# Kernel tuning notes

Measured on AMD Instinct MI355X. Metric: run time of the kernel, lower is better.

The kernel has to match this reference:

```python
import jax, jax.numpy as jnp
import numpy as np
import math

N_EMBD = 1024
N_HEADS = 16
B, T = 4, 2048

def setup_inputs() -> dict:
    key = jax.random.key(0)
    k1, k2, k3 = jax.random.split(key, 3)
    x = jax.random.normal(k1, (B, T, N_EMBD), dtype=jnp.float32)
    scale = 1.0 / math.sqrt(N_EMBD)
    W_attn = jax.random.normal(k2, (N_EMBD, 3 * N_EMBD), dtype=jnp.float32) * scale
    W_proj = jax.random.normal(k3, (N_EMBD, N_EMBD), dtype=jnp.float32) * scale
    return {"x": x, "W_attn": W_attn, "W_proj": W_proj}

def reference(x, W_attn, W_proj):
    Bb, Tt, C = x.shape
    hd = C // N_HEADS
    qkv = x @ W_attn  # [B,T,3C]
    q, k, v = jnp.split(qkv, 3, axis=-1)
    # [B,H,T,hd]
    q = q.reshape(Bb, Tt, N_HEADS, hd).transpose(0, 2, 1, 3)
    k = k.reshape(Bb, Tt, N_HEADS, hd).transpose(0, 2, 1, 3)
    v = v.reshape(Bb, Tt, N_HEADS, hd).transpose(0, 2, 1, 3)
    att = jnp.einsum('bhqd,bhkd->bhqk', q, k) * (1.0 / math.sqrt(hd))
    mask = jnp.tril(jnp.ones((Tt, Tt), dtype=bool))
    att = jnp.where(mask[None, None], att, -jnp.inf)
    att = jax.nn.softmax(att, axis=-1)
    out = jnp.einsum('bhqk,bhkd->bhqd', att, v)
    out = out.transpose(0, 2, 1, 3).reshape(Bb, Tt, C)
    return out @ W_proj
```

## Files before the change

kernel.cpp:

```cpp
#include <hip/hip_runtime.h>
#include <cstddef>
#include <cstdint>

typedef __attribute__((ext_vector_type(8))) _Float16 half8;
typedef __attribute__((ext_vector_type(4))) _Float16 half4;
typedef __attribute__((ext_vector_type(4))) float f32x4;
typedef __attribute__((ext_vector_type(16))) float f32x16;

#define N_EMBD 1024
#define N_HEADS 16
#define BATCH 4
#define SEQ 2048
#define C3 3072
#define HD 64

__device__ inline uint32_t pk2(float x, float y) {
    auto h2 = __builtin_amdgcn_cvt_pkrtz(x, y);
    uint32_t u;
    __builtin_memcpy(&u, &h2, 4);
    return u;
}

__device__ inline void swap32(uint32_t& a, uint32_t& b) {
    asm volatile("v_permlane32_swap_b32 %0, %1" : "+v"(a), "+v"(b));
}

__device__ inline float exp2_hw(float x) {
    float r;
    asm("v_exp_f32 %0, %1" : "=v"(r) : "v"(x));
    return r;
}

__device__ inline void transpose_tile(const float* __restrict__ in, _Float16* __restrict__ out,
                                      int R, int Ncols, int bx, int by, int tx, int ty,
                                      int scale_below, float scl) {
    __shared__ float tile[32][33];
    int n0 = bx * 32, r0 = by * 32;
#pragma unroll
    for (int i = 0; i < 32; i += 8)
        tile[ty + i][tx] = in[(size_t)(r0 + ty + i) * Ncols + n0 + tx];
    __syncthreads();
#pragma unroll
    for (int i = 0; i < 32; i += 8) {
        int orow = n0 + ty + i;
        float f = tile[tx][ty + i];
        if (orow < scale_below) f *= scl;
        out[(size_t)orow * R + r0 + tx] = (_Float16)f;
    }
}

__global__ void prep_kernel(const float* __restrict__ x, _Float16* __restrict__ xh,
                            const float* __restrict__ Wa, _Float16* __restrict__ WaT,
                            const float* __restrict__ Wp, _Float16* __restrict__ WpT) {
    const int bid = blockIdx.x;
    const int tx = threadIdx.x & 31, ty = threadIdx.x >> 5;
    const float qscale = 0.125f * 1.44269504089f;
    if (bid < 8192) {
        int i = (bid * 256 + threadIdx.x) * 4;
        float4 v = *(const float4*)(x + i);
        half4 h;
        h[0] = (_Float16)v.x; h[1] = (_Float16)v.y; h[2] = (_Float16)v.z; h[3] = (_Float16)v.w;
        *(half4*)(xh + i) = h;
    } else if (bid < 8192 + 3072) {
        int v = bid - 8192;
        transpose_tile(Wa, WaT, N_EMBD, C3, v % 96, v / 96, tx, ty, N_EMBD, qscale);
    } else {
        int v = bid - 8192 - 3072;
        transpose_tile(Wp, WpT, N_EMBD, N_EMBD, v % 32, v / 32, tx, ty, 0, 1.0f);
    }
}

__global__ void transpose_v(const _Float16* __restrict__ qkv, _Float16* __restrict__ vT) {
    __shared__ _Float16 tile[32][36];
    int t0 = blockIdx.x * 32;
    int bhd = blockIdx.y;
    int bh = bhd >> 1, dh = bhd & 1;
    int b = bh >> 4, h = bh & 15;
    int tx = threadIdx.x, ty = threadIdx.y;
#pragma unroll
    for (int i = 0; i < 32; i += 8)
        tile[ty + i][tx] = qkv[(size_t)(b * SEQ + t0 + ty + i) * C3 + 2 * N_EMBD + h * HD + dh * 32 + tx];
    __syncthreads();
#pragma unroll
    for (int i = 0; i < 32; i += 8)
        vT[((size_t)bh * HD + dh * 32 + ty + i) * SEQ + t0 + tx] = tile[tx][ty + i];
}

__device__ inline void store1(float* p, float v) { *p = v; }
__device__ inline void store1(_Float16* p, float v) { *p = (_Float16)v; }

__global__ __launch_bounds__(512, 1) void gemm192(
    const _Float16* __restrict__ A, const _Float16* __restrict__ Bt,
    _Float16* __restrict__ C, _Float16* __restrict__ vT, int M, int N, int K) {
    __shared__ _Float16 smem[2 * 256 * 64 + 2 * 192 * 64];
    _Float16* Al0 = smem;
    _Float16* Bl0 = smem + 2 * 256 * 64;
    const int tid = threadIdx.x;
    const int lane = tid & 63, wave = tid >> 6;
    const int l15 = lane & 15, l4 = lane >> 4;
    const int wm = wave >> 2, wn = wave & 3;

    const int nwg = gridDim.x, nbx = N / 192;
    int wg = blockIdx.x;
    if ((nwg & 7) == 0) { int cpx = nwg >> 3; wg = (wg & 7) * cpx + (wg >> 3); }
    const int row0 = (wg / nbx) * 256, col0 = (wg % nbx) * 192;
    const int TAU = K >> 6;

    const int srow = tid >> 3, su = tid & 7;
    const int usrc8 = (su ^ (srow & 7)) * 8;
    auto stageAu = [&](int unit, int ts) {
        __builtin_amdgcn_global_load_lds(
            (const __attribute__((address_space(1))) void*)(A + (size_t)(row0 + unit * 64 + srow) * K + ts * 64 + usrc8),
            (__attribute__((address_space(3))) void*)(Al0 + (ts & 1) * 16384 + unit * 4096 + tid * 8), 16, 0, 0);
    };
    auto stageBu = [&](int unit, int ts) {
        __builtin_amdgcn_global_load_lds(
            (const __attribute__((address_space(1))) void*)(Bt + (size_t)(col0 + unit * 64 + srow) * K + ts * 64 + usrc8),
            (__attribute__((address_space(3))) void*)(Bl0 + (ts & 1) * 12288 + unit * 4096 + tid * 8), 16, 0, 0);
    };
    auto stageTile = [&](int ts) {
        stageAu(0, ts); stageAu(1, ts); stageAu(2, ts); stageAu(3, ts);
        stageBu(0, ts); stageBu(1, ts); stageBu(2, ts);
    };

    f32x4 acc[8][3] = {};
    stageTile(0); stageTile(1);
    asm volatile("s_waitcnt vmcnt(7)" ::: "memory");
    __builtin_amdgcn_s_barrier();

    half8 a[4][2], b[3][2];
    for (int tau = 0; tau < TAU; ++tau) {
        const _Float16* Ab = Al0 + (tau & 1) * 16384;
        const _Float16* Bb = Bl0 + (tau & 1) * 12288;
        const bool t2 = (tau + 2 < TAU);

#pragma unroll
        for (int m = 0; m < 4; ++m)
#pragma unroll
            for (int ks = 0; ks < 2; ++ks) {
                int r = wm * 128 + m * 16 + l15;
                a[m][ks] = *(const half8*)(Ab + r * 64 + (((ks * 4 + l4) ^ (r & 7)) * 8));
            }
#pragma unroll
        for (int n = 0; n < 3; ++n)
#pragma unroll
            for (int ks = 0; ks < 2; ++ks) {
                int r = wn * 48 + n * 16 + l15;
                b[n][ks] = *(const half8*)(Bb + r * 64 + (((ks * 4 + l4) ^ (r & 7)) * 8));
            }
        __builtin_amdgcn_s_barrier();
        __builtin_amdgcn_s_setprio(1);
#pragma unroll
        for (int m = 0; m < 4; ++m)
#pragma unroll
            for (int n = 0; n < 2; ++n)
#pragma unroll
                for (int ks = 0; ks < 2; ++ks)
                    acc[m][n] = __builtin_amdgcn_mfma_f32_16x16x32_f16(a[m][ks], b[n][ks], acc[m][n], 0, 0, 0);
        __builtin_amdgcn_s_setprio(0);
        __builtin_amdgcn_s_barrier();

        if (t2) { stageBu(0, tau + 2); stageBu(1, tau + 2); stageBu(2, tau + 2); }
        __builtin_amdgcn_s_barrier();
        __builtin_amdgcn_s_setprio(1);
#pragma unroll
        for (int m = 0; m < 4; ++m)
#pragma unroll
            for (int ks = 0; ks < 2; ++ks)
                acc[m][2] = __builtin_amdgcn_mfma_f32_16x16x32_f16(a[m][ks], b[2][ks], acc[m][2], 0, 0, 0);
        __builtin_amdgcn_s_setprio(0);
        __builtin_amdgcn_s_barrier();

#pragma unroll
        for (int m = 0; m < 4; ++m)
#pragma unroll
            for (int ks = 0; ks < 2; ++ks) {
                int r = wm * 128 + 64 + m * 16 + l15;
                a[m][ks] = *(const half8*)(Ab + r * 64 + (((ks * 4 + l4) ^ (r & 7)) * 8));
            }
        if (t2) { stageAu(0, tau + 2); stageAu(2, tau + 2); }
        __builtin_amdgcn_s_barrier();
        __builtin_amdgcn_s_setprio(1);
#pragma unroll
        for (int m = 0; m < 4; ++m)
#pragma unroll
            for (int n = 0; n < 2; ++n)
#pragma unroll
                for (int ks = 0; ks < 2; ++ks)
                    acc[4 + m][n] = __builtin_amdgcn_mfma_f32_16x16x32_f16(a[m][ks], b[n][ks], acc[4 + m][n], 0, 0, 0);
        __builtin_amdgcn_s_setprio(0);
        __builtin_amdgcn_s_barrier();

        if (t2) { stageAu(1, tau + 2); stageAu(3, tau + 2); }
        __builtin_amdgcn_s_barrier();
        __builtin_amdgcn_s_setprio(1);
#pragma unroll
        for (int m = 0; m < 4; ++m)
#pragma unroll
            for (int ks = 0; ks < 2; ++ks)
                acc[4 + m][2] = __builtin_amdgcn_mfma_f32_16x16x32_f16(a[m][ks], b[2][ks], acc[4 + m][2], 0, 0, 0);
        __builtin_amdgcn_s_setprio(0);
        if (tau <= TAU - 3) {
            asm volatile("s_waitcnt vmcnt(7)" ::: "memory");
        } else if (tau == TAU - 2) {
            asm volatile("s_waitcnt vmcnt(0)" ::: "memory");
        }
        __builtin_amdgcn_s_barrier();
    }

    const int vlo = 2 * N_EMBD;
    const bool fuseV = (vT != nullptr) && (col0 + 192 > vlo);
    _Float16* vbuf = smem;
#pragma unroll
    for (int mi = 0; mi < 8; ++mi)
#pragma unroll
        for (int ni = 0; ni < 3; ++ni) {
            int c = col0 + wn * 48 + ni * 16 + l15;
            int rb = wm * 128 + (mi >> 2) * 64 + (mi & 3) * 16 + l4 * 4;
            if ((vT != nullptr) && c >= vlo) {
                if (fuseV) {
                    half4 hv;
#pragma unroll
                    for (int j = 0; j < 4; ++j) hv[j] = (_Float16)acc[mi][ni][j];
                    *(half4*)(&vbuf[(c - col0) * 264 + rb]) = hv;
                }
            } else {
#pragma unroll
                for (int j = 0; j < 4; ++j)
                    store1(C + (size_t)(row0 + rb + j) * N + c, acc[mi][ni][j]);
            }
        }
    if (fuseV) {
        __syncthreads();
        const int vc0 = (col0 > vlo) ? col0 : vlo;
        const int W = col0 + 192 - vc0;
        const int nch = W * 32;
        const int bB = row0 >> 11;
        const int t0 = row0 & 2047;
        for (int ch = tid; ch < nch; ch += 512) {
            int crow = ch >> 5, ck = ch & 31;
            int c = vc0 + crow;
            half8 hv = *(const half8*)(&vbuf[(c - col0) * 264 + ck * 8]);
            int hh = (c - vlo) >> 6, dd = (c - vlo) & 63;
            *(half8*)(&vT[((size_t)(bB * 16 + hh) * 64 + dd) * SEQ + t0 + ck * 8]) = hv;
        }
    }
}

template <typename OutT>
__global__ __launch_bounds__(256, 2) void gemm_h(
    const _Float16* __restrict__ A, const _Float16* __restrict__ Bt,
    OutT* __restrict__ C, int M, int N, int K) {
    __shared__ _Float16 Al[3][128 * 32];
    __shared__ _Float16 Bl[3][128 * 32];
    const int tid = threadIdx.x;
    const int wave = tid >> 6, lane = tid & 63;
    const int l15 = lane & 15, l4 = lane >> 4;
    const int gx = gridDim.x;
    int lin = blockIdx.y * gx + blockIdx.x;
    int bcol, brow;
    if ((gx & 7) == 0) {
        int cpx = gx >> 3;
        int xcd = lin & 7;
        int idx = lin >> 3;
        bcol = xcd * cpx + idx % cpx;
        brow = idx / cpx;
    } else { bcol = blockIdx.x; brow = blockIdx.y; }
    const int row0 = brow * 128, col0 = bcol * 128;
    const int wm = wave >> 1, wn = wave & 1;
    const int TAU = K >> 5;

    auto stageT = [&](int ts, int buf) {
#pragma unroll
        for (int i = 0; i < 2; ++i) {
            int c = tid + 256 * i;
            int r = c >> 2, c8 = (c & 3) * 8;
            __builtin_amdgcn_global_load_lds(
                (const __attribute__((address_space(1))) void*)(A + (size_t)(row0 + r) * K + ts * 32 + c8),
                (__attribute__((address_space(3))) void*)(&Al[buf][(size_t)(wave * 64 + 256 * i) * 8]),
                16, 0, 0);
        }
#pragma unroll
        for (int i = 0; i < 2; ++i) {
            int c = tid + 256 * i;
            int r = c >> 2, c8 = (c & 3) * 8;
            __builtin_amdgcn_global_load_lds(
                (const __attribute__((address_space(1))) void*)(Bt + (size_t)(col0 + r) * K + ts * 32 + c8),
                (__attribute__((address_space(3))) void*)(&Bl[buf][(size_t)(wave * 64 + 256 * i) * 8]),
                16, 0, 0);
        }
    };

    f32x4 acc[4][4] = {};
    stageT(0, 0); stageT(1, 1);
    asm volatile("s_waitcnt vmcnt(4)" ::: "memory");
    __builtin_amdgcn_s_barrier();

    int cur = 0;
    for (int t = 0; t < TAU; ++t) {
        int sb = cur + 2; if (sb >= 3) sb -= 3;
        if (t + 2 < TAU) stageT(t + 2, sb);
        half8 a[4], b[4];
#pragma unroll
        for (int m = 0; m < 4; ++m)
            a[m] = *(const half8*)(&Al[cur][(wm * 64 + m * 16 + l15) * 32 + l4 * 8]);
#pragma unroll
        for (int n = 0; n < 4; ++n)
            b[n] = *(const half8*)(&Bl[cur][(wn * 64 + n * 16 + l15) * 32 + l4 * 8]);
        __builtin_amdgcn_s_setprio(1);
#pragma unroll
        for (int m = 0; m < 4; ++m)
#pragma unroll
            for (int n = 0; n < 4; ++n)
                acc[m][n] = __builtin_amdgcn_mfma_f32_16x16x32_f16(a[m], b[n], acc[m][n], 0, 0, 0);
        __builtin_amdgcn_s_setprio(0);
        if (t + 2 < TAU) {
            asm volatile("s_waitcnt vmcnt(4)" ::: "memory");
        } else if (t + 1 < TAU) {
            asm volatile("s_waitcnt vmcnt(0)" ::: "memory");
        }
        __builtin_amdgcn_s_barrier();
        ++cur; if (cur == 3) cur = 0;
    }
#pragma unroll
    for (int m = 0; m < 4; ++m)
#pragma unroll
        for (int n = 0; n < 4; ++n)
#pragma unroll
            for (int j = 0; j < 4; ++j) {
                int r = row0 + wm * 64 + m * 16 + l4 * 4 + j;
                int cc = col0 + wn * 64 + n * 16 + l15;
                store1(C + (size_t)r * N + cc, acc[m][n][j]);
            }
}

__global__ __launch_bounds__(256, 3) void attn_kernel(const _Float16* __restrict__ qkv,
                                                      const _Float16* __restrict__ vT,
                                                      _Float16* __restrict__ ao) {
    const int bid = blockIdx.x;
    const int pairp = bid >> 6;
    const int bh = bid & 63;
    const int b = bh >> 4, h = bh & 15;
    const int tid = threadIdx.x, lane = tid & 63;
    const int wave = tid >> 6;
    const int l31 = lane & 31, L = lane >> 5;

    __shared__ _Float16 Kl[3][64 * 64];
    __shared__ _Float16 Vl[3][64 * 64];
    __shared__ float l_s[4][32];

    const float NEGC = -4.0f * 1.44269504089f;

    auto stage = [&](int t, int buf) {
#pragma unroll
        for (int i = 0; i < 2; ++i) {
            int idx = tid + 256 * i;
            int key = idx >> 3;
            int d8 = ((idx & 7) ^ (key & 7)) * 8;
            __builtin_amdgcn_global_load_lds(
                (const __attribute__((address_space(1))) void*)(qkv + (size_t)(b * SEQ + t * 64 + key) * C3 + N_EMBD + h * HD + d8),
                (__attribute__((address_space(3))) void*)(&Kl[buf][idx * 8]), 16, 0, 0);
        }
#pragma unroll
        for (int i = 0; i < 2; ++i) {
            int idx = tid + 256 * i;
            int d = idx >> 3;
            int k8 = ((idx & 7) ^ (d & 7)) * 8;
            __builtin_amdgcn_global_load_lds(
                (const __attribute__((address_space(1))) void*)(vT + ((size_t)bh * HD + d) * SEQ + t * 64 + k8),
                (__attribute__((address_space(3))) void*)(&Vl[buf][idx * 8]), 16, 0, 0);
        }
    };

    const f32x16 cinit = (f32x16)(NEGC);

    for (int pass = 0; pass < 2; ++pass) {
        const int qt = pass ? (15 - pairp) : pairp;
        const int q0w = qt * 128 + wave * 32;
        const int q_g = q0w + l31;
        const int nt = 2 * qt + 2;

        stage(0, 0);
        stage(1, 1);

        half8 qb[4];
#pragma unroll
        for (int ks = 0; ks < 4; ++ks)
            qb[ks] = *(const half8*)(qkv + (size_t)(b * SEQ + q_g) * C3 + h * HD + ks * 16 + L * 8);

        f32x16 o[2];
        o[0] = (f32x16)(0.f);
        o[1] = (f32x16)(0.f);
        float ls0 = 0.f, ls1 = 0.f, ls2 = 0.f, ls3 = 0.f;

        asm volatile("s_waitcnt vmcnt(4)" ::: "memory");
        __builtin_amdgcn_s_barrier();

        int cur = 0;
        for (int t = 0; t < nt; ++t) {
            const int kv0 = t * 64;
            int sb = cur + 2; if (sb >= 3) sb -= 3;
            if (t + 2 < nt) stage(t + 2, sb);

            if (kv0 <= q0w + 31) {
                const _Float16* Kb = &Kl[cur][0];
                const _Float16* Vb = &Vl[cur][0];
                f32x16 s[2];
                __builtin_amdgcn_s_setprio(1);
#pragma unroll
                for (int kb = 0; kb < 2; ++kb) {
                    const int key = kb * 32 + l31;
                    {
                        half8 kf = *(const half8*)(Kb + key * 64 + ((L ^ (key & 7)) * 8));
                        s[kb] = __builtin_amdgcn_mfma_f32_32x32x16_f16(kf, qb[0], cinit, 0, 0, 0);
                    }
#pragma unroll
                    for (int ks = 1; ks < 4; ++ks) {
                        half8 kf = *(const half8*)(Kb + key * 64 + (((ks * 2 + L) ^ (key & 7)) * 8));
                        s[kb] = __builtin_amdgcn_mfma_f32_32x32x16_f16(kf, qb[ks], s[kb], 0, 0, 0);
                    }
                }
                __builtin_amdgcn_s_setprio(0);
                const bool needmask = (kv0 + 63 > q0w);
#pragma unroll
                for (int kb = 0; kb < 2; ++kb) {
#pragma unroll
                    for (int r = 0; r < 16; ++r) {
                        float v = exp2_hw(s[kb][r]);
                        if (needmask) {
                            int key_g = kv0 + kb * 32 + (r & 3) + 8 * (r >> 2) + 4 * L;
                            v = (key_g > q_g) ? 0.f : v;
                        }
                        s[kb][r] = v;
                        if ((r & 3) == 0) ls0 += v;
                        else if ((r & 3) == 1) ls1 += v;
                        else if ((r & 3) == 2) ls2 += v;
                        else ls3 += v;
                    }
                }
                half8 paf[4];
#pragma unroll
                for (int kb = 0; kb < 2; ++kb)
#pragma unroll
                    for (int hf = 0; hf < 2; ++hf) {
                        const int bse = hf * 8;
                        uint32_t a0 = pk2(s[kb][bse + 0], s[kb][bse + 1]);
                        uint32_t b0 = pk2(s[kb][bse + 4], s[kb][bse + 5]);
                        swap32(a0, b0);
                        uint32_t a1 = pk2(s[kb][bse + 2], s[kb][bse + 3]);
                        uint32_t b1 = pk2(s[kb][bse + 6], s[kb][bse + 7]);
                        swap32(a1, b1);
                        uint32_t w[4] = {a0, a1, b0, b1};
                        __builtin_memcpy(&paf[kb * 2 + hf], w, 16);
                    }
                __builtin_amdgcn_s_setprio(1);
#pragma unroll
                for (int ks = 0; ks < 4; ++ks) {
#pragma unroll
                    for (int db = 0; db < 2; ++db) {
                        const int d = db * 32 + l31;
                        half8 vb = *(const half8*)(Vb + d * 64 + (((ks * 2 + L) ^ (d & 7)) * 8));
                        o[db] = __builtin_amdgcn_mfma_f32_32x32x16_f16(paf[ks], vb, o[db], 0, 0, 0);
                    }
                }
                __builtin_amdgcn_s_setprio(0);
            }

            if (t + 2 < nt) {
                asm volatile("s_waitcnt vmcnt(4)" ::: "memory");
            } else if (t + 1 < nt) {
                asm volatile("s_waitcnt vmcnt(0)" ::: "memory");
            }
            __builtin_amdgcn_s_barrier();
            ++cur; if (cur == 3) cur = 0;
        }

        float lrow = (ls0 + ls1) + (ls2 + ls3);
        lrow += __shfl_xor(lrow, 32, 64);
        l_s[wave][l31] = lrow;
        asm volatile("s_waitcnt lgkmcnt(0)" ::: "memory");
        __builtin_amdgcn_sched_barrier(0);
        float lq[16];
#pragma unroll
        for (int r = 0; r < 16; ++r)
            lq[r] = l_s[wave][(r & 3) + 8 * (r >> 2) + 4 * L];
        asm volatile("s_waitcnt lgkmcnt(0)" ::: "memory");
        __builtin_amdgcn_sched_barrier(0);
#pragma unroll
        for (int db = 0; db < 2; ++db)
#pragma unroll
            for (int r = 0; r < 16; ++r) {
                int qg = q0w + (r & 3) + 8 * (r >> 2) + 4 * L;
                ao[(size_t)(b * SEQ + qg) * N_EMBD + h * HD + db * 32 + l31] =
                    (_Float16)(o[db][r] / lq[r]);
            }
    }
}

extern "C" void kernel_launch(void* const* d_in, const int* in_sizes, int n_in,
                              void* d_out, int out_size, void* d_ws, size_t ws_size,
                              hipStream_t stream) {
    const float* x  = (const float*)d_in[0];
    const float* Wa = (const float*)d_in[1];
    const float* Wp = (const float*)d_in[2];
    float* out = (float*)d_out;

    const int M = BATCH * SEQ;
    _Float16* xh  = (_Float16*)d_ws;
    _Float16* WaT = xh + (size_t)M * N_EMBD;
    _Float16* WpT = WaT + (size_t)C3 * N_EMBD;
    _Float16* qkv = WpT + (size_t)N_EMBD * N_EMBD;
    _Float16* ao  = qkv + (size_t)M * C3;
    _Float16* vTn = ao + (size_t)M * N_EMBD;

    const size_t need = ((size_t)M * N_EMBD * 3 + (size_t)C3 * N_EMBD +
                         (size_t)N_EMBD * N_EMBD + (size_t)M * C3) * sizeof(_Float16);
    const bool fused = (ws_size >= need);
    _Float16* vT = fused ? vTn : xh;

    prep_kernel<<<dim3(8192 + 3072 + 1024), 256, 0, stream>>>(x, xh, Wa, WaT, Wp, WpT);

    gemm192<<<dim3((M / 256) * (C3 / 192)), 512, 0, stream>>>(
        xh, WaT, qkv, fused ? vT : nullptr, M, C3, N_EMBD);

    if (!fused) {
        dim3 tb(32, 8);
        transpose_v<<<dim3(SEQ / 32, BATCH * N_HEADS * 2), tb, 0, stream>>>(qkv, vT);
    }

    attn_kernel<<<dim3(512), 256, 0, stream>>>(qkv, vT, ao);

    gemm_h<float><<<dim3(N_EMBD / 128, M / 128), 256, 0, stream>>>(ao, WpT, out, M, N_EMBD, N_EMBD);
}
```

Before: 168.1 us.

## Software-pipeline attention loop so QK of next tile overlaps softmax/PV of previous

```diff
diff --git a/kernel.cpp b/kernel.cpp
--- a/kernel.cpp
+++ b/kernel.cpp
@@ -351,7 +351,7 @@
 
     const float NEGC = -4.0f * 1.44269504089f;
 
-    auto stage = [&](int t, int buf) {
+    auto stageK = [&](int t, int buf) {
 #pragma unroll
         for (int i = 0; i < 2; ++i) {
             int idx = tid + 256 * i;
@@ -361,6 +361,8 @@
                 (const __attribute__((address_space(1))) void*)(qkv + (size_t)(b * SEQ + t * 64 + key) * C3 + N_EMBD + h * HD + d8),
                 (__attribute__((address_space(3))) void*)(&Kl[buf][idx * 8]), 16, 0, 0);
         }
+    };
+    auto stageV = [&](int t, int buf) {
 #pragma unroll
         for (int i = 0; i < 2; ++i) {
             int idx = tid + 256 * i;
@@ -380,8 +382,9 @@
         const int q_g = q0w + l31;
         const int nt = 2 * qt + 2;
 
-        stage(0, 0);
-        stage(1, 1);
+        stageV(0, 0);
+        stageK(0, 0);
+        stageK(1, 1);
 
         half8 qb[4];
 #pragma unroll
@@ -392,88 +395,110 @@
         o[0] = (f32x16)(0.f);
         o[1] = (f32x16)(0.f);
         float ls0 = 0.f, ls1 = 0.f, ls2 = 0.f, ls3 = 0.f;
+        f32x16 sE[2], sO[2];
+
+        auto qk = [&](int t, f32x16 (&s)[2], int buf) {
+            if (t * 64 > q0w + 31) return;
+            const _Float16* Kb = &Kl[buf][0];
+            __builtin_amdgcn_s_setprio(1);
+#pragma unroll
+            for (int kb = 0; kb < 2; ++kb) {
+                const int key = kb * 32 + l31;
+                {
+                    half8 kf = *(const half8*)(Kb + key * 64 + ((L ^ (key & 7)) * 8));
+                    s[kb] = __builtin_amdgcn_mfma_f32_32x32x16_f16(kf, qb[0], cinit, 0, 0, 0);
+                }
+#pragma unroll
+                for (int ks = 1; ks < 4; ++ks) {
+                    half8 kf = *(const half8*)(Kb + key * 64 + (((ks * 2 + L) ^ (key & 7)) * 8));
+                    s[kb] = __builtin_amdgcn_mfma_f32_32x32x16_f16(kf, qb[ks], s[kb], 0, 0, 0);
+                }
+            }
+            __builtin_amdgcn_s_setprio(0);
+        };
+
+        auto finish = [&](int t, f32x16 (&s)[2], int buf) {
+            if (t * 64 > q0w + 31) return;
+            const int kv0 = t * 64;
+            const _Float16* Vb = &Vl[buf][0];
+            const bool needmask = (kv0 + 63 > q0w);
+#pragma unroll
+            for (int kb = 0; kb < 2; ++kb) {
+#pragma unroll
+                for (int r = 0; r < 16; ++r) {
+                    float v = exp2_hw(s[kb][r]);
+                    if (needmask) {
+                        int key_g = kv0 + kb * 32 + (r & 3) + 8 * (r >> 2) + 4 * L;
+                        v = (key_g > q_g) ? 0.f : v;
+                    }
+                    s[kb][r] = v;
+                    if ((r & 3) == 0) ls0 += v;
+                    else if ((r & 3) == 1) ls1 += v;
+                    else if ((r & 3) == 2) ls2 += v;
+                    else ls3 += v;
+                }
+            }
+            half8 paf[4];
+#pragma unroll
+            for (int kb = 0; kb < 2; ++kb)
+#pragma unroll
+                for (int hf = 0; hf < 2; ++hf) {
+                    const int bse = hf * 8;
+                    uint32_t a0 = pk2(s[kb][bse + 0], s[kb][bse + 1]);
+                    uint32_t b0 = pk2(s[kb][bse + 4], s[kb][bse + 5]);
+                    swap32(a0, b0);
+                    uint32_t a1 = pk2(s[kb][bse + 2], s[kb][bse + 3]);
+                    uint32_t b1 = pk2(s[kb][bse + 6], s[kb][bse + 7]);
+                    swap32(a1, b1);
+                    uint32_t w[4] = {a0, a1, b0, b1};
+                    __builtin_memcpy(&paf[kb * 2 + hf], w, 16);
+                }
+            __builtin_amdgcn_s_setprio(1);
+#pragma unroll
+            for (int ks = 0; ks < 4; ++ks) {
+#pragma unroll
+                for (int db = 0; db < 2; ++db) {
+                    const int d = db * 32 + l31;
+                    half8 vb = *(const half8*)(Vb + d * 64 + (((ks * 2 + L) ^ (d & 7)) * 8));
+                    o[db] = __builtin_amdgcn_mfma_f32_32x32x16_f16(paf[ks], vb, o[db], 0, 0, 0);
+                }
+            }
+            __builtin_amdgcn_s_setprio(0);
+        };
 
         asm volatile("s_waitcnt vmcnt(4)" ::: "memory");
         __builtin_amdgcn_s_barrier();
 
-        int cur = 0;
-        for (int t = 0; t < nt; ++t) {
-            const int kv0 = t * 64;
-            int sb = cur + 2; if (sb >= 3) sb -= 3;
-            if (t + 2 < nt) stage(t + 2, sb);
-
-            if (kv0 <= q0w + 31) {
-                const _Float16* Kb = &Kl[cur][0];
-                const _Float16* Vb = &Vl[cur][0];
-                f32x16 s[2];
-                __builtin_amdgcn_s_setprio(1);
-#pragma unroll
-                for (int kb = 0; kb < 2; ++kb) {
-                    const int key = kb * 32 + l31;
-                    {
-                        half8 kf = *(const half8*)(Kb + key * 64 + ((L ^ (key & 7)) * 8));
-                        s[kb] = __builtin_amdgcn_mfma_f32_32x32x16_f16(kf, qb[0], cinit, 0, 0, 0);
-                    }
-#pragma unroll
-                    for (int ks = 1; ks < 4; ++ks) {
-                        half8 kf = *(const half8*)(Kb + key * 64 + (((ks * 2 + L) ^ (key & 7)) * 8));
-                        s[kb] = __builtin_amdgcn_mfma_f32_32x32x16_f16(kf, qb[ks], s[kb], 0, 0, 0);
-                    }
-                }
-                __builtin_amdgcn_s_setprio(0);
-                const bool needmask = (kv0 + 63 > q0w);
-#pragma unroll
-                for (int kb = 0; kb < 2; ++kb) {
-#pragma unroll
-                    for (int r = 0; r < 16; ++r) {
-                        float v = exp2_hw(s[kb][r]);
-                        if (needmask) {
-                            int key_g = kv0 + kb * 32 + (r & 3) + 8 * (r >> 2) + 4 * L;
-                            v = (key_g > q_g) ? 0.f : v;
-                        }
-                        s[kb][r] = v;
-                        if ((r & 3) == 0) ls0 += v;
-                        else if ((r & 3) == 1) ls1 += v;
-                        else if ((r & 3) == 2) ls2 += v;
-                        else ls3 += v;
-                    }
-                }
-                half8 paf[4];
-#pragma unroll
-                for (int kb = 0; kb < 2; ++kb)
-#pragma unroll
-                    for (int hf = 0; hf < 2; ++hf) {
-                        const int bse = hf * 8;
-                        uint32_t a0 = pk2(s[kb][bse + 0], s[kb][bse + 1]);
-                        uint32_t b0 = pk2(s[kb][bse + 4], s[kb][bse + 5]);
-                        swap32(a0, b0);
-                        uint32_t a1 = pk2(s[kb][bse + 2], s[kb][bse + 3]);
-                        uint32_t b1 = pk2(s[kb][bse + 6], s[kb][bse + 7]);
-                        swap32(a1, b1);
-                        uint32_t w[4] = {a0, a1, b0, b1};
-                        __builtin_memcpy(&paf[kb * 2 + hf], w, 16);
-                    }
-                __builtin_amdgcn_s_setprio(1);
-#pragma unroll
-                for (int ks = 0; ks < 4; ++ks) {
-#pragma unroll
-                    for (int db = 0; db < 2; ++db) {
-                        const int d = db * 32 + l31;
-                        half8 vb = *(const half8*)(Vb + d * 64 + (((ks * 2 + L) ^ (d & 7)) * 8));
-                        o[db] = __builtin_amdgcn_mfma_f32_32x32x16_f16(paf[ks], vb, o[db], 0, 0, 0);
-                    }
-                }
-                __builtin_amdgcn_s_setprio(0);
-            }
-
-            if (t + 2 < nt) {
+        stageV(1, 1);
+        if (2 < nt) stageK(2, 2);
+        qk(0, sE, 0);
+        asm volatile("s_waitcnt vmcnt(4)" ::: "memory");
+        __builtin_amdgcn_s_barrier();
+
+        int u = 1;
+        for (; u + 2 < nt; u += 2) {
+            stageV(u + 1, (u + 1) % 3);
+            stageK(u + 2, (u + 2) % 3);
+            qk(u, sO, u % 3);
+            finish(u - 1, sE, (u - 1) % 3);
+            asm volatile("s_waitcnt vmcnt(4)" ::: "memory");
+            __builtin_amdgcn_s_barrier();
+            stageV(u + 2, (u + 2) % 3);
+            if (u + 3 < nt) stageK(u + 3, (u + 3) % 3);
+            qk(u + 1, sE, (u + 1) % 3);
+            finish(u, sO, u % 3);
+            if (u + 3 < nt) {
                 asm volatile("s_waitcnt vmcnt(4)" ::: "memory");
-            } else if (t + 1 < nt) {
-                asm volatile("s_waitcnt vmcnt(0)" ::: "memory");
+            } else {
+                asm volatile("s_waitcnt vmcnt(2)" ::: "memory");
             }
             __builtin_amdgcn_s_barrier();
-            ++cur; if (cur == 3) cur = 0;
-        }
+        }
+        qk(nt - 1, sO, (nt - 1) % 3);
+        finish(nt - 2, sE, (nt - 2) % 3);
+        asm volatile("s_waitcnt vmcnt(0)" ::: "memory");
+        __builtin_amdgcn_s_barrier();
+        finish(nt - 1, sO, (nt - 1) % 3);
 
         float lrow = (ls0 + ls1) + (ls2 + ls3);
         lrow += __shfl_xor(lrow, 32, 64);
@@ -494,6 +519,7 @@
                 ao[(size_t)(b * SEQ + qg) * N_EMBD + h * HD + db * 32 + l31] =
                     (_Float16)(o[db][r] / lq[r]);
             }
+        __builtin_amdgcn_s_barrier();
     }
 }
 
```

New measurement: 218.3 us. 29.9% more time.
